# Optimization experiments

Hardware: AMD Instinct MI355X
Metric: run time of the kernel (lower is better)

The kernel has to match this reference:

```python
import math
import jax, jax.numpy as jnp
import numpy as np

B, SQ, SK, D, H = 4, 2048, 2048, 1024, 16
HD = D // H  # 64


def setup_inputs() -> dict:
    key = jax.random.key(0)
    k1, k2, k3, k4, k5 = jax.random.split(key, 5)
    scale = 1.0 / math.sqrt(D)
    return {
        "hidden_states": jax.random.normal(k1, (B, SQ, D), dtype=jnp.float32),
        "encoder_hidden_states": jax.random.normal(k2, (B, SK, D), dtype=jnp.float32),
        "Wq": jax.random.normal(k3, (D, D), dtype=jnp.float32) * scale,
        "Wk": jax.random.normal(k4, (D, D), dtype=jnp.float32) * scale,
        "Wv": jax.random.normal(k5, (D, D), dtype=jnp.float32) * scale,
    }


def reference(hidden_states, encoder_hidden_states, Wq, Wk, Wv):
    # Linear (bias=False): y = x @ W^T, then split heads -> [B, H, S, HD]
    def split_heads(x, S):
        return x.reshape(B, S, H, HD).transpose(0, 2, 1, 3)

    q = split_heads(hidden_states @ Wq.T, SQ)
    k = split_heads(encoder_hidden_states @ Wk.T, SK)
    v = split_heads(encoder_hidden_states @ Wv.T, SK)

    scores = jnp.einsum("bhqd,bhkd->bhqk", q, k) / math.sqrt(HD)
    probs = jax.nn.softmax(scores, axis=-1)  # no mask, dropout p=0
    ctx = jnp.einsum("bhqk,bhkd->bhqd", probs, v)
    # merge heads -> [B, SQ, D]
    return ctx.transpose(0, 2, 1, 3).reshape(B, SQ, D)
```

## Files before the change

### kernel.cpp

```cpp
#include <hip/hip_runtime.h>
#include <hip/hip_bf16.h>

typedef unsigned short u16;
typedef unsigned int u32;
typedef __attribute__((ext_vector_type(8))) short bf16x8;
typedef __attribute__((ext_vector_type(4))) float f32x4;

#define MFMA32(a, b, c) __builtin_amdgcn_mfma_f32_16x16x32_bf16(a, b, c, 0, 0, 0)

__device__ __forceinline__ float fexp2(float x) { return __builtin_amdgcn_exp2f(x); }

__device__ __forceinline__ u16 f2bf(float f) {
  u32 u = __float_as_uint(f);
  u += 0x7fffu + ((u >> 16) & 1u);
  return (u16)(u >> 16);
}
__device__ __forceinline__ u32 pack2rn(float a, float b) {
  return (u32)f2bf(a) | ((u32)f2bf(b) << 16);
}
__device__ __forceinline__ bf16x8 cvt8(const float4 a, const float4 b) {
  union { bf16x8 v; u32 p[4]; } r;
  r.p[0] = pack2rn(a.x, a.y); r.p[1] = pack2rn(a.z, a.w);
  r.p[2] = pack2rn(b.x, b.y); r.p[3] = pack2rn(b.z, b.w);
  return r.v;
}

__device__ __forceinline__ u32 cvtpk(float lo, float hi) {
  u32 r;
  asm("v_cvt_pk_bf16_f32 %0, %1, %2" : "=v"(r) : "v"(lo), "v"(hi));
  return r;
}
__device__ __forceinline__ void pl32swap(u32& a, u32& b) {
  asm("v_permlane32_swap_b32 %0, %1" : "+v"(a), "+v"(b));
}
__device__ __forceinline__ void pl16swap(u32& a, u32& b) {
  asm("v_permlane16_swap_b32 %0, %1" : "+v"(a), "+v"(b));
}

__device__ __forceinline__ void async_copy16(const void* g, void* l) {
  __builtin_amdgcn_global_load_lds(
      (const __attribute__((address_space(1))) unsigned int*)g,
      (__attribute__((address_space(3))) unsigned int*)l, 16, 0, 0);
}

__global__ __launch_bounds__(256) void cvt_bf16(
    const float* __restrict__ s0, const float* __restrict__ s1,
    const float* __restrict__ s2, const float* __restrict__ s3,
    const float* __restrict__ s4,
    u16* __restrict__ d0, u16* __restrict__ d1, u16* __restrict__ d2,
    u16* __restrict__ d3, u16* __restrict__ d4) {
  const int z = blockIdx.z;
  const float* s = (z == 0) ? s0 : (z == 1) ? s1 : (z == 2) ? s2 : (z == 3) ? s3 : s4;
  u16* d = (z == 0) ? d0 : (z == 1) ? d1 : (z == 2) ? d2 : (z == 3) ? d3 : d4;
  const int n8 = ((z < 2) ? (8192 * 1024) : (1024 * 1024)) / 8;
  const int stride = gridDim.x * 256;
  for (int i = blockIdx.x * 256 + threadIdx.x; i < n8; i += stride) {
    const float4 a = *(const float4*)(s + (size_t)i * 8);
    const float4 b = *(const float4*)(s + (size_t)i * 8 + 4);
    *(bf16x8*)(d + (size_t)i * 8) = cvt8(a, b);
  }
}

__global__ __launch_bounds__(256) void proj_gemm_bf(
    const u16* __restrict__ hb, const u16* __restrict__ eb,
    const u16* __restrict__ wb,
    u16* __restrict__ qb, u16* __restrict__ kb, u16* __restrict__ vt) {
  const int z = blockIdx.z;
  const u16* Ag = (z == 0) ? hb : eb;
  const u16* Bg = wb + (size_t)z * 1024 * 1024;
  const int m0 = blockIdx.y * 128;
  const int n0 = blockIdx.x * 128;
  __shared__ __attribute__((aligned(16))) u16 Al[128 * 32];
  __shared__ __attribute__((aligned(16))) u16 Bl[128 * 32];
  const int tid = threadIdx.x;
  const int w = tid >> 6, lane = tid & 63;
  const int wm = w >> 1, wn = w & 1;
  const int l15 = lane & 15, quad = lane >> 4;
  const int srow = lane >> 2, sch = lane & 3;

  f32x4 acc[4][4] = {};

  for (int k0 = 0; k0 < 1024; k0 += 32) {
    __syncthreads();
#pragma unroll
    for (int j = 0; j < 2; j++) {
      const int row = w * 32 + j * 16 + srow;
      async_copy16(Ag + (size_t)(m0 + row) * 1024 + k0 + sch * 8,
                   &Al[(w * 32 + j * 16) * 32]);
      async_copy16(Bg + (size_t)(n0 + row) * 1024 + k0 + sch * 8,
                   &Bl[(w * 32 + j * 16) * 32]);
    }
    __syncthreads();
    bf16x8 af[4], bfr[4];
#pragma unroll
    for (int t = 0; t < 4; t++) {
      af[t] = *(const bf16x8*)&Al[(wm * 64 + t * 16 + l15) * 32 + quad * 8];
      bfr[t] = *(const bf16x8*)&Bl[(wn * 64 + t * 16 + l15) * 32 + quad * 8];
    }
#pragma unroll
    for (int mt = 0; mt < 4; mt++)
#pragma unroll
      for (int nt = 0; nt < 4; nt++)
        acc[mt][nt] = MFMA32(af[mt], bfr[nt], acc[mt][nt]);
  }

  if (z < 2) {
    u16* C = (z == 0) ? qb : kb;
    const float sc = (z == 0) ? 0.18033688011112042f : 1.0f;
#pragma unroll
    for (int mt = 0; mt < 4; mt++)
#pragma unroll
      for (int nt = 0; nt < 4; nt++) {
        const int col = n0 + wn * 64 + nt * 16 + l15;
#pragma unroll
        for (int rr = 0; rr < 4; rr++) {
          const int rowm = m0 + wm * 64 + mt * 16 + quad * 4 + rr;
          C[(size_t)rowm * 1024 + col] = f2bf(acc[mt][nt][rr] * sc);
        }
      }
  } else {
    const int b = m0 >> 11;
#pragma unroll
    for (int mt = 0; mt < 4; mt++) {
      const int key = (m0 & 2047) + wm * 64 + mt * 16 + quad * 4;
#pragma unroll
      for (int nt = 0; nt < 4; nt++) {
        const int n = n0 + wn * 64 + nt * 16 + l15;
        const int h = n >> 6, hd = n & 63;
        uint2 v;
        v.x = pack2rn(acc[mt][nt][0], acc[mt][nt][1]);
        v.y = pack2rn(acc[mt][nt][2], acc[mt][nt][3]);
        *(uint2*)&vt[((size_t)((b * 16 + h) * 64 + hd)) * 2048 + key] = v;
      }
    }
  }
}

__global__ __launch_bounds__(256) void proj_gemm_f32(
    const float* __restrict__ hs, const float* __restrict__ ehs,
    const float* __restrict__ wq, const float* __restrict__ wk,
    const float* __restrict__ wv,
    u16* __restrict__ qb, u16* __restrict__ kb, u16* __restrict__ vt) {
  const int z = blockIdx.z;
  const float* Ag = (z == 0) ? hs : ehs;
  const float* Bg = (z == 0) ? wq : ((z == 1) ? wk : wv);
  const int m0 = blockIdx.y * 128;
  const int n0 = blockIdx.x * 128;
  __shared__ __attribute__((aligned(16))) u16 Al[128 * 40];
  __shared__ __attribute__((aligned(16))) u16 Bl[128 * 40];
  const int tid = threadIdx.x;
  const int w = tid >> 6, lane = tid & 63;
  const int wm = w >> 1, wn = w & 1;
  const int l15 = lane & 15, quad = lane >> 4;
  const int srow = lane >> 2, sch = lane & 3;
  const int r0 = w * 32 + srow, r1 = r0 + 16;

  const float* Ap0 = Ag + (size_t)(m0 + r0) * 1024 + sch * 8;
  const float* Ap1 = Ag + (size_t)(m0 + r1) * 1024 + sch * 8;
  const float* Bp0 = Bg + (size_t)(n0 + r0) * 1024 + sch * 8;
  const float* Bp1 = Bg + (size_t)(n0 + r1) * 1024 + sch * 8;

  f32x4 acc[4][4] = {};

  for (int k0 = 0; k0 < 1024; k0 += 32) {
    const float4 a0l = *(const float4*)(Ap0 + k0), a0h = *(const float4*)(Ap0 + k0 + 4);
    const float4 a1l = *(const float4*)(Ap1 + k0), a1h = *(const float4*)(Ap1 + k0 + 4);
    const float4 b0l = *(const float4*)(Bp0 + k0), b0h = *(const float4*)(Bp0 + k0 + 4);
    const float4 b1l = *(const float4*)(Bp1 + k0), b1h = *(const float4*)(Bp1 + k0 + 4);
    __syncthreads();
    *(bf16x8*)&Al[r0 * 40 + sch * 8] = cvt8(a0l, a0h);
    *(bf16x8*)&Al[r1 * 40 + sch * 8] = cvt8(a1l, a1h);
    *(bf16x8*)&Bl[r0 * 40 + sch * 8] = cvt8(b0l, b0h);
    *(bf16x8*)&Bl[r1 * 40 + sch * 8] = cvt8(b1l, b1h);
    __syncthreads();
    bf16x8 af[4], bfr[4];
#pragma unroll
    for (int t = 0; t < 4; t++) {
      af[t] = *(const bf16x8*)&Al[(wm * 64 + t * 16 + l15) * 40 + quad * 8];
      bfr[t] = *(const bf16x8*)&Bl[(wn * 64 + t * 16 + l15) * 40 + quad * 8];
    }
#pragma unroll
    for (int mt = 0; mt < 4; mt++)
#pragma unroll
      for (int nt = 0; nt < 4; nt++)
        acc[mt][nt] = MFMA32(af[mt], bfr[nt], acc[mt][nt]);
  }

  if (z < 2) {
    u16* C = (z == 0) ? qb : kb;
    const float sc = (z == 0) ? 0.18033688011112042f : 1.0f;
#pragma unroll
    for (int mt = 0; mt < 4; mt++)
#pragma unroll
      for (int nt = 0; nt < 4; nt++) {
        const int col = n0 + wn * 64 + nt * 16 + l15;
#pragma unroll
        for (int rr = 0; rr < 4; rr++) {
          const int rowm = m0 + wm * 64 + mt * 16 + quad * 4 + rr;
          C[(size_t)rowm * 1024 + col] = f2bf(acc[mt][nt][rr] * sc);
        }
      }
  } else {
    const int b = m0 >> 11;
#pragma unroll
    for (int mt = 0; mt < 4; mt++) {
      const int key = (m0 & 2047) + wm * 64 + mt * 16 + quad * 4;
#pragma unroll
      for (int nt = 0; nt < 4; nt++) {
        const int n = n0 + wn * 64 + nt * 16 + l15;
        const int h = n >> 6, hd = n & 63;
        uint2 v;
        v.x = pack2rn(acc[mt][nt][0], acc[mt][nt][1]);
        v.y = pack2rn(acc[mt][nt][2], acc[mt][nt][3]);
        *(uint2*)&vt[((size_t)((b * 16 + h) * 64 + hd)) * 2048 + key] = v;
      }
    }
  }
}

__global__ __launch_bounds__(256, 3) void attn_fwd(
    const u16* __restrict__ qb, const u16* __restrict__ kb,
    const u16* __restrict__ vt, float* __restrict__ out) {
  const int bh = blockIdx.y;
  const int b = bh >> 4, h = bh & 15;
  const int q0 = blockIdx.x * 128;
  const int tid = threadIdx.x;
  const int w = tid >> 6, lane = tid & 63;
  const int l15 = lane & 15, quad = lane >> 4;

  __shared__ __attribute__((aligned(16))) u16 Kl[2][64 * 64];
  __shared__ __attribute__((aligned(16))) u16 Vl[2][64 * 64];

  const int wq = w * 32;
  bf16x8 qf[2][2];
#pragma unroll
  for (int nt = 0; nt < 2; nt++)
#pragma unroll
    for (int ks = 0; ks < 2; ks++)
      qf[nt][ks] = *(const bf16x8*)&qb[((size_t)(b * 2048 + q0 + wq + nt * 16 + l15)) * 1024 +
                                       h * 64 + ks * 32 + quad * 8];

  f32x4 o[4][2] = {};
  f32x4 lacc[2] = {};
  const f32x4 z4 = {0.f, 0.f, 0.f, 0.f};
  union { bf16x8 v; u32 p[4]; } one_;
  one_.p[0] = one_.p[1] = one_.p[2] = one_.p[3] = 0x3F803F80u;
  const bf16x8 ones = one_.v;

  const int rsw = (l15 & 7) << 3;
  const int lr = lane >> 3;
  const int cs8 = ((lane & 7) ^ lr) * 8;
  const u16* Kp = kb + ((size_t)(b * 2048 + w * 16 + lr)) * 1024 + h * 64 + cs8;
  const u16* Vp = vt + ((size_t)((b * 16 + h) * 64 + w * 16 + lr)) * 2048 + cs8;

#pragma unroll
  for (int j = 0; j < 2; j++) {
    async_copy16(Kp + (size_t)j * 8 * 1024, &Kl[0][(w * 16 + j * 8) * 64]);
    async_copy16(Vp + (size_t)j * 8 * 2048, &Vl[0][(w * 16 + j * 8) * 64]);
  }

  for (int t = 0; t < 32; ++t) {
    const int cur = t & 1;
    __syncthreads();
    if (t < 31) {
      const size_t ko = (size_t)(t + 1) * 64;
#pragma unroll
      for (int j = 0; j < 2; j++) {
        async_copy16(Kp + (ko + (size_t)j * 8) * 1024,
                     &Kl[cur ^ 1][(w * 16 + j * 8) * 64]);
        async_copy16(Vp + (size_t)j * 8 * 2048 + ko,
                     &Vl[cur ^ 1][(w * 16 + j * 8) * 64]);
      }
    }
    const u16* Kc = Kl[cur];
    const u16* Vc = Vl[cur];

    f32x4 s[4][2];
#pragma unroll
    for (int mt = 0; mt < 4; mt++) {
      const bf16x8 kf = *(const bf16x8*)&Kc[(mt * 16 + l15) * 64 + ((quad * 8) ^ rsw)];
      s[mt][0] = MFMA32(kf, qf[0][0], z4);
      s[mt][1] = MFMA32(kf, qf[1][0], z4);
    }
#pragma unroll
    for (int mt = 0; mt < 4; mt++) {
      const bf16x8 kf =
          *(const bf16x8*)&Kc[(mt * 16 + l15) * 64 + ((32 + quad * 8) ^ rsw)];
      s[mt][0] = MFMA32(kf, qf[0][1], s[mt][0]);
      s[mt][1] = MFMA32(kf, qf[1][1], s[mt][1]);
    }

#pragma unroll
    for (int mt = 0; mt < 4; mt++)
#pragma unroll
      for (int nt = 0; nt < 2; nt++)
#pragma unroll
        for (int rr = 0; rr < 4; rr++)
          s[mt][nt][rr] = fexp2(s[mt][nt][rr]);

#pragma unroll
    for (int kt = 0; kt < 2; kt++) {
      bf16x8 pf[2];
#pragma unroll
      for (int nt = 0; nt < 2; nt++) {
        u32 r00 = cvtpk(s[2 * kt][nt][0], s[2 * kt][nt][1]);
        u32 r01 = cvtpk(s[2 * kt][nt][2], s[2 * kt][nt][3]);
        u32 r10 = cvtpk(s[2 * kt + 1][nt][0], s[2 * kt + 1][nt][1]);
        u32 r11 = cvtpk(s[2 * kt + 1][nt][2], s[2 * kt + 1][nt][3]);
        pl32swap(r00, r10);
        pl32swap(r01, r11);
        pl16swap(r00, r10);
        pl16swap(r01, r11);
        union { bf16x8 v; u32 p[4]; } u;
        u.p[0] = r00; u.p[1] = r01; u.p[2] = r10; u.p[3] = r11;
        pf[nt] = u.v;
      }
      lacc[0] = MFMA32(ones, pf[0], lacc[0]);
      lacc[1] = MFMA32(ones, pf[1], lacc[1]);
#pragma unroll
      for (int ht = 0; ht < 4; ht++) {
        const bf16x8 vf =
            *(const bf16x8*)&Vc[(ht * 16 + l15) * 64 + ((kt * 32 + quad * 8) ^ rsw)];
        o[ht][0] = MFMA32(vf, pf[0], o[ht][0]);
        o[ht][1] = MFMA32(vf, pf[1], o[ht][1]);
      }
    }
  }

#pragma unroll
  for (int nt = 0; nt < 2; nt++) {
    const float rl = 1.0f / lacc[nt][0];
    const size_t rowOff = ((size_t)(b * 2048 + q0 + wq + nt * 16 + l15)) * 1024 + h * 64;
#pragma unroll
    for (int ht = 0; ht < 4; ht++) {
      float4 v;
      v.x = o[ht][nt][0] * rl;
      v.y = o[ht][nt][1] * rl;
      v.z = o[ht][nt][2] * rl;
      v.w = o[ht][nt][3] * rl;
      *(float4*)&out[rowOff + ht * 16 + quad * 4] = v;
    }
  }
}

extern "C" void kernel_launch(void* const* d_in, const int* in_sizes, int n_in,
                              void* d_out, int out_size, void* d_ws, size_t ws_size,
                              hipStream_t stream) {
  const float* hs  = (const float*)d_in[0];
  const float* ehs = (const float*)d_in[1];
  const float* wqp = (const float*)d_in[2];
  const float* wkp = (const float*)d_in[3];
  const float* wvp = (const float*)d_in[4];
  const size_t M8 = (size_t)8192 * 1024;
  u16* qb = (u16*)d_ws;
  u16* kb = qb + M8;
  u16* vt = kb + M8;
  float* ob = (float*)d_out;

  const size_t need = (3 * M8 + 2 * M8 + 3 * (size_t)1024 * 1024) * 2;
  if (ws_size >= need) {
    u16* hb = vt + M8;
    u16* eb = hb + M8;
    u16* wb = eb + M8;
    dim3 gc(512, 1, 5);
    cvt_bf16<<<gc, dim3(256), 0, stream>>>(hs, ehs, wqp, wkp, wvp,
                                           hb, eb, wb, wb + M8 / 8, wb + M8 / 4);
    dim3 gg(8, 64, 3);
    proj_gemm_bf<<<gg, dim3(256), 0, stream>>>(hb, eb, wb, qb, kb, vt);
  } else {
    dim3 gg(8, 64, 3);
    proj_gemm_f32<<<gg, dim3(256), 0, stream>>>(hs, ehs, wqp, wkp, wvp, qb, kb, vt);
  }
  dim3 ga(16, 64, 1);
  attn_fwd<<<ga, dim3(256), 0, stream>>>(qb, kb, vt, ob);
}
```

Before: 277.3 us.

## Double GEMM K-tile with XOR-swizzled LDS and XCD-aware block remapping

The projection GEMM now stages a 64-wide K slice per iteration instead of 32, which halves the number of barrier pairs. Its LDS layout uses an XOR swizzle to avoid bank conflicts on the fragment reads. Both the GEMM and attention kernels switch to 1D grids whose block index is remapped so that consecutive blocks on the same XCD share A/B rows or K/V heads, improving L2 locality. The larger tile doubles LDS use, which may reduce occupancy.

New measurement: 249.4 us. -10.1%, faster.

```diff
diff --git a/kernel.cpp b/kernel.cpp
--- a/kernel.cpp
+++ b/kernel.cpp
@@ -65,43 +65,53 @@
     const u16* __restrict__ hb, const u16* __restrict__ eb,
     const u16* __restrict__ wb,
     u16* __restrict__ qb, u16* __restrict__ kb, u16* __restrict__ vt) {
-  const int z = blockIdx.z;
+  const int lin = blockIdx.x;
+  const int swz = (lin & 7) * 192 + (lin >> 3);
+  const int z = swz >> 9;
+  const int rem = swz & 511;
+  const int m0 = (rem >> 3) * 128;
+  const int n0 = (rem & 7) * 128;
   const u16* Ag = (z == 0) ? hb : eb;
   const u16* Bg = wb + (size_t)z * 1024 * 1024;
-  const int m0 = blockIdx.y * 128;
-  const int n0 = blockIdx.x * 128;
-  __shared__ __attribute__((aligned(16))) u16 Al[128 * 32];
-  __shared__ __attribute__((aligned(16))) u16 Bl[128 * 32];
+  __shared__ __attribute__((aligned(16))) u16 Al[128 * 64];
+  __shared__ __attribute__((aligned(16))) u16 Bl[128 * 64];
   const int tid = threadIdx.x;
   const int w = tid >> 6, lane = tid & 63;
   const int wm = w >> 1, wn = w & 1;
   const int l15 = lane & 15, quad = lane >> 4;
-  const int srow = lane >> 2, sch = lane & 3;
+  const int lr = lane >> 3;
+  const int cs8 = ((lane & 7) ^ lr) * 8;
+  const int rsw = (l15 & 7) << 3;
+
+  const u16* Ap = Ag + (size_t)(m0 + w * 32 + lr) * 1024 + cs8;
+  const u16* Bp = Bg + (size_t)(n0 + w * 32 + lr) * 1024 + cs8;
 
   f32x4 acc[4][4] = {};
 
-  for (int k0 = 0; k0 < 1024; k0 += 32) {
-    __syncthreads();
-#pragma unroll
-    for (int j = 0; j < 2; j++) {
-      const int row = w * 32 + j * 16 + srow;
-      async_copy16(Ag + (size_t)(m0 + row) * 1024 + k0 + sch * 8,
-                   &Al[(w * 32 + j * 16) * 32]);
-      async_copy16(Bg + (size_t)(n0 + row) * 1024 + k0 + sch * 8,
-                   &Bl[(w * 32 + j * 16) * 32]);
-    }
-    __syncthreads();
-    bf16x8 af[4], bfr[4];
-#pragma unroll
-    for (int t = 0; t < 4; t++) {
-      af[t] = *(const bf16x8*)&Al[(wm * 64 + t * 16 + l15) * 32 + quad * 8];
-      bfr[t] = *(const bf16x8*)&Bl[(wn * 64 + t * 16 + l15) * 32 + quad * 8];
-    }
-#pragma unroll
-    for (int mt = 0; mt < 4; mt++)
-#pragma unroll
-      for (int nt = 0; nt < 4; nt++)
-        acc[mt][nt] = MFMA32(af[mt], bfr[nt], acc[mt][nt]);
+  for (int k0 = 0; k0 < 1024; k0 += 64) {
+    __syncthreads();
+#pragma unroll
+    for (int j = 0; j < 4; j++) {
+      async_copy16(Ap + (size_t)j * 8 * 1024 + k0, &Al[(w * 32 + j * 8) * 64]);
+      async_copy16(Bp + (size_t)j * 8 * 1024 + k0, &Bl[(w * 32 + j * 8) * 64]);
+    }
+    __syncthreads();
+#pragma unroll
+    for (int ks = 0; ks < 2; ks++) {
+      bf16x8 af[4], bfr[4];
+#pragma unroll
+      for (int t = 0; t < 4; t++) {
+        af[t] = *(const bf16x8*)&Al[(wm * 64 + t * 16 + l15) * 64 +
+                                    ((ks * 32 + quad * 8) ^ rsw)];
+        bfr[t] = *(const bf16x8*)&Bl[(wn * 64 + t * 16 + l15) * 64 +
+                                     ((ks * 32 + quad * 8) ^ rsw)];
+      }
+#pragma unroll
+      for (int mt = 0; mt < 4; mt++)
+#pragma unroll
+        for (int nt = 0; nt < 4; nt++)
+          acc[mt][nt] = MFMA32(af[mt], bfr[nt], acc[mt][nt]);
+    }
   }
 
   if (z < 2) {
@@ -221,9 +231,11 @@
 __global__ __launch_bounds__(256, 3) void attn_fwd(
     const u16* __restrict__ qb, const u16* __restrict__ kb,
     const u16* __restrict__ vt, float* __restrict__ out) {
-  const int bh = blockIdx.y;
+  const int lin = blockIdx.x;
+  const int swz = (lin & 7) * 128 + (lin >> 3);
+  const int bh = swz >> 4;
   const int b = bh >> 4, h = bh & 15;
-  const int q0 = blockIdx.x * 128;
+  const int q0 = (swz & 15) * 128;
   const int tid = threadIdx.x;
   const int w = tid >> 6, lane = tid & 63;
   const int l15 = lane & 15, quad = lane >> 4;
@@ -365,12 +377,10 @@
     dim3 gc(512, 1, 5);
     cvt_bf16<<<gc, dim3(256), 0, stream>>>(hs, ehs, wqp, wkp, wvp,
                                            hb, eb, wb, wb + M8 / 8, wb + M8 / 4);
-    dim3 gg(8, 64, 3);
-    proj_gemm_bf<<<gg, dim3(256), 0, stream>>>(hb, eb, wb, qb, kb, vt);
+    proj_gemm_bf<<<dim3(1536), dim3(256), 0, stream>>>(hb, eb, wb, qb, kb, vt);
   } else {
     dim3 gg(8, 64, 3);
     proj_gemm_f32<<<gg, dim3(256), 0, stream>>>(hs, ehs, wqp, wkp, wvp, qb, kb, vt);
   }
-  dim3 ga(16, 64, 1);
-  attn_fwd<<<ga, dim3(256), 0, stream>>>(qb, kb, vt, ob);
-}
+  attn_fwd<<<dim3(1024), dim3(256), 0, stream>>>(qb, kb, vt, ob);
+}
```
